# Optimization experiments

Measured on AMD Instinct MI355X. Metric: run time of the kernel, lower is better.

The kernel has to match this reference:

```python
import jax, jax.numpy as jnp
import numpy as np

B, I, H = 4096, 1024, 2048
EPS = 1e-5  # nn.GroupNorm default eps


def setup_inputs() -> dict:
    key = jax.random.key(0)
    ks = jax.random.split(key, 16)
    s_in = 1.0 / np.sqrt(I)
    s_h = 1.0 / np.sqrt(H)
    inp = {
        "x": jax.random.normal(ks[0], (B, I), jnp.float32),
        "h_prev": jax.random.normal(ks[1], (B, H), jnp.float32),
        "c_prev": jax.random.normal(ks[2], (B, H), jnp.float32),
        "n_prev": jnp.ones((B, H), jnp.float32),
        "m_prev": jax.random.normal(ks[3], (B, H), jnp.float32),
        # W_* : Linear(I, H) weight [H, I] + bias [H]
        "Wi": jax.random.uniform(ks[4], (H, I), jnp.float32, -s_in, s_in),
        "Wf": jax.random.uniform(ks[5], (H, I), jnp.float32, -s_in, s_in),
        "Wz": jax.random.uniform(ks[6], (H, I), jnp.float32, -s_in, s_in),
        "Wo": jax.random.uniform(ks[7], (H, I), jnp.float32, -s_in, s_in),
        "bi": jax.random.uniform(ks[8], (H,), jnp.float32, -s_in, s_in),
        "bf": jax.random.uniform(ks[9], (H,), jnp.float32, -s_in, s_in),
        "bz": jax.random.uniform(ks[10], (H,), jnp.float32, -s_in, s_in),
        "bo": jax.random.uniform(ks[11], (H,), jnp.float32, -s_in, s_in),
        # R_* : Linear(H, H, bias=False) weight [H, H]
        "Ri": jax.random.uniform(ks[12], (H, H), jnp.float32, -s_h, s_h),
        "Rf": jax.random.uniform(ks[13], (H, H), jnp.float32, -s_h, s_h),
        "Rz": jax.random.uniform(ks[14], (H, H), jnp.float32, -s_h, s_h),
        "Ro": jax.random.uniform(ks[15], (H, H), jnp.float32, -s_h, s_h),
        # GroupNorm(1, H) affine params
        "gn_w": jnp.ones((H,), jnp.float32),
        "gn_b": jnp.zeros((H,), jnp.float32),
    }
    return inp


def _group_norm1(x, w, b):
    # GroupNorm with 1 group on [B, H]: normalize over all H per sample
    mu = jnp.mean(x, axis=-1, keepdims=True)
    var = jnp.mean(jnp.square(x - mu), axis=-1, keepdims=True)
    return (x - mu) * jax.lax.rsqrt(var + EPS) * w + b


def reference(x, h_prev, c_prev, n_prev, m_prev,
              Wi, Wf, Wz, Wo, bi, bf, bz, bo,
              Ri, Rf, Rz, Ro, gn_w, gn_b):
    # Batch the 4 input and 4 recurrent GEMMs into one each: [B, 4H]
    Wcat = jnp.concatenate([Wi, Wf, Wz, Wo], axis=0)   # [4H, I]
    bcat = jnp.concatenate([bi, bf, bz, bo], axis=0)   # [4H]
    Rcat = jnp.concatenate([Ri, Rf, Rz, Ro], axis=0)   # [4H, H]
    pre = x @ Wcat.T + bcat + h_prev @ Rcat.T          # [B, 4H]
    pi, pf, pz, po = jnp.split(pre, 4, axis=-1)
    i = jax.nn.sigmoid(pi)
    f = jax.nn.sigmoid(pf)
    z = jnp.tanh(pz)
    o = jax.nn.sigmoid(po)
    m = jnp.maximum(f * m_prev, i)
    c = f * c_prev + i * z
    n = f * n_prev + i
    c_stab = c / n
    h = o * jnp.tanh(_group_norm1(c_stab, gn_w, gn_b))
    return (h, c, n, m)
```

## Files before the change

### kernel.cpp

```cpp
#include <hip/hip_runtime.h>
#include <hip/hip_bf16.h>
#include <math.h>

#define B_ 4096
#define I_ 1024
#define H_ 2048
#define K_ 3072
#define N4 8192
#define EPSGN 1e-5f

#define NT_K 48
#define PANB 16384
#define LDSB 65536

typedef __bf16 bf16;
typedef __bf16 bf16x8 __attribute__((ext_vector_type(8)));
typedef float  f32x4  __attribute__((ext_vector_type(4)));

__device__ __forceinline__ float sigm(float x) {
  return 1.0f / (1.0f + __expf(-x));
}
__device__ __forceinline__ float tanh_fast(float x) {
  float a = fabsf(x);
  float e = __expf(-2.0f * a);
  float t = (1.0f - e) / (1.0f + e);
  return copysignf(t, x);
}

__global__ void convA(const float* __restrict__ x, const float* __restrict__ hp,
                      char* __restrict__ At) {
  int sid = blockIdx.x * blockDim.x + threadIdx.x;
  int p = sid & 1023;
  int pan = sid >> 10;
  int mt = pan / 96;
  int rem = pan - mt * 96;
  int kt = rem >> 1;
  int h = rem & 1;
  int r = p >> 3;
  int ks = (p & 7) ^ (r & 7);
  int row = mt * 256 + h * 128 + r;
  int k = kt * 64 + ks * 8;
  const float* src = (k < I_) ? (x + (size_t)row * I_ + k)
                              : (hp + (size_t)row * H_ + (k - I_));
  f32x4 v0 = *(const f32x4*)src;
  f32x4 v1 = *(const f32x4*)(src + 4);
  bf16x8 o;
  o[0]=(bf16)v0[0]; o[1]=(bf16)v0[1]; o[2]=(bf16)v0[2]; o[3]=(bf16)v0[3];
  o[4]=(bf16)v1[0]; o[5]=(bf16)v1[1]; o[6]=(bf16)v1[2]; o[7]=(bf16)v1[3];
  *(bf16x8*)(At + (size_t)sid * 16) = o;
}

__global__ void convB(const float* __restrict__ Wi, const float* __restrict__ Wf,
                      const float* __restrict__ Wz, const float* __restrict__ Wo,
                      const float* __restrict__ Ri, const float* __restrict__ Rf,
                      const float* __restrict__ Rz, const float* __restrict__ Ro,
                      char* __restrict__ Bt) {
  int sid = blockIdx.x * blockDim.x + threadIdx.x;
  int p = sid & 1023;
  int pan = sid >> 10;
  int nt = pan / 96;
  int rem = pan - nt * 96;
  int kt = rem >> 1;
  int h = rem & 1;
  int r = p >> 3;
  int ks = (p & 7) ^ (r & 7);
  int n = nt * 256 + h * 128 + r;
  int g = n >> 11;
  int hr = n & 2047;
  int k = kt * 64 + ks * 8;
  const float* Wp = (g == 0) ? Wi : (g == 1) ? Wf : (g == 2) ? Wz : Wo;
  const float* Rp = (g == 0) ? Ri : (g == 1) ? Rf : (g == 2) ? Rz : Ro;
  const float* src = (k < I_) ? (Wp + (size_t)hr * I_ + k)
                              : (Rp + (size_t)hr * H_ + (k - I_));
  f32x4 v0 = *(const f32x4*)src;
  f32x4 v1 = *(const f32x4*)(src + 4);
  bf16x8 o;
  o[0]=(bf16)v0[0]; o[1]=(bf16)v0[1]; o[2]=(bf16)v0[2]; o[3]=(bf16)v0[3];
  o[4]=(bf16)v1[0]; o[5]=(bf16)v1[1]; o[6]=(bf16)v1[2]; o[7]=(bf16)v1[3];
  *(bf16x8*)(Bt + (size_t)sid * 16) = o;
}

__device__ __forceinline__ void gload16(const char* g, char* l) {
  __builtin_amdgcn_global_load_lds(
      (const __attribute__((address_space(1))) void*)g,
      (__attribute__((address_space(3))) void*)l, 16, 0, 0);
}
__device__ __forceinline__ void stage(const char* g, char* l) {
  gload16(g, l);
  gload16(g + 8192, l + 8192);
}

__global__ __launch_bounds__(512, 2) void gemm8(const char* __restrict__ At,
                                                const char* __restrict__ Bt,
                                                bf16* __restrict__ pre) {
  extern __shared__ char lds[];
  const int tid = threadIdx.x;
  const int lane = tid & 63;
  const int wv = tid >> 6;
  const int wm = wv >> 2;
  const int wn = wv & 3;

  int bid = (blockIdx.x & 7) * 64 + (blockIdx.x >> 3);
  const int bm = bid >> 5;
  const int bn = bid & 31;

  const char* a_src = At + (size_t)bm * (NT_K * 2 * PANB) + tid * 16;
  const char* b_src = Bt + (size_t)bn * (NT_K * 2 * PANB) + tid * 16;
  char* a_lds = lds + tid * 16;
  char* b_lds = lds + LDSB + tid * 16;

  const int l15 = lane & 15;
  const int l7  = lane & 7;
  const int q   = lane >> 4;
  int offk[2];
  offk[0] = l15 * 128 + (((0 + q) ^ l7) << 4);
  offk[1] = l15 * 128 + (((4 + q) ^ l7) << 4);

  const char* apan_base = lds + wm * PANB;
  const char* bpan_base = lds + LDSB + (wn >> 1) * PANB;
  const int bcol = (wn & 1) * 8192;

  f32x4 acc[8][4] = {};
  bf16x8 af[4][2], bfr[2][2][2];

  stage(b_src + 0 * PANB, b_lds + 0 * PANB);
  stage(b_src + 1 * PANB, b_lds + 1 * PANB);
  stage(a_src + 0 * PANB, a_lds + 0 * PANB);
  stage(a_src + 1 * PANB, a_lds + 1 * PANB);
  stage(b_src + 2 * PANB, b_lds + 2 * PANB);
  stage(b_src + 3 * PANB, b_lds + 3 * PANB);
  asm volatile("s_waitcnt vmcnt(4)" ::: "memory");
  __builtin_amdgcn_s_barrier();

#pragma unroll 2
  for (int t = 0; t < NT_K; ++t) {
    const int par = (t & 1) * 2;
    const char* apan = apan_base + par * PANB;
    const char* bpan = bpan_base + par * PANB;

#pragma unroll
    for (int fi = 0; fi < 4; ++fi)
#pragma unroll
      for (int ks = 0; ks < 2; ++ks)
        af[fi][ks] = *(const bf16x8*)(apan + fi * 2048 + offk[ks]);
#pragma unroll
    for (int fj = 0; fj < 2; ++fj)
#pragma unroll
      for (int ks = 0; ks < 2; ++ks)
        bfr[0][fj][ks] = *(const bf16x8*)(bpan + bcol + fj * 2048 + offk[ks]);
    if (t + 1 < NT_K)
      stage(a_src + (size_t)(t + 1) * 2 * PANB,
            a_lds + (((t + 1) & 1) * 2) * PANB);
    __builtin_amdgcn_s_barrier();
    asm volatile("s_waitcnt lgkmcnt(0)" ::: "memory");
    __builtin_amdgcn_s_setprio(1);
#pragma unroll
    for (int fi = 0; fi < 4; ++fi)
#pragma unroll
      for (int fj = 0; fj < 2; ++fj)
#pragma unroll
        for (int ks = 0; ks < 2; ++ks)
          acc[fi][fj] = __builtin_amdgcn_mfma_f32_16x16x32_bf16(
              af[fi][ks], bfr[0][fj][ks], acc[fi][fj], 0, 0, 0);
    __builtin_amdgcn_s_setprio(0);
    __builtin_amdgcn_s_barrier();

#pragma unroll
    for (int fj = 0; fj < 2; ++fj)
#pragma unroll
      for (int ks = 0; ks < 2; ++ks)
        bfr[1][fj][ks] = *(const bf16x8*)(bpan + bcol + 4096 + fj * 2048 + offk[ks]);
    if (t + 1 < NT_K)
      stage(a_src + (size_t)(t + 1) * 2 * PANB + PANB,
            a_lds + ((((t + 1) & 1) * 2) + 1) * PANB);
    __builtin_amdgcn_s_barrier();
    asm volatile("s_waitcnt lgkmcnt(0)" ::: "memory");
    __builtin_amdgcn_s_setprio(1);
#pragma unroll
    for (int fi = 0; fi < 4; ++fi)
#pragma unroll
      for (int fj = 0; fj < 2; ++fj)
#pragma unroll
        for (int ks = 0; ks < 2; ++ks)
          acc[fi][2 + fj] = __builtin_amdgcn_mfma_f32_16x16x32_bf16(
              af[fi][ks], bfr[1][fj][ks], acc[fi][2 + fj], 0, 0, 0);
    __builtin_amdgcn_s_setprio(0);
    __builtin_amdgcn_s_barrier();

#pragma unroll
    for (int fi = 0; fi < 4; ++fi)
#pragma unroll
      for (int ks = 0; ks < 2; ++ks)
        af[fi][ks] = *(const bf16x8*)(apan + 8192 + fi * 2048 + offk[ks]);
    if (t + 2 < NT_K)
      stage(b_src + (size_t)(t + 2) * 2 * PANB,
            b_lds + par * PANB);
    __builtin_amdgcn_s_barrier();
    asm volatile("s_waitcnt lgkmcnt(0)" ::: "memory");
    __builtin_amdgcn_s_setprio(1);
#pragma unroll
    for (int fi = 0; fi < 4; ++fi)
#pragma unroll
      for (int fj = 0; fj < 2; ++fj)
#pragma unroll
        for (int ks = 0; ks < 2; ++ks)
          acc[4 + fi][2 + fj] = __builtin_amdgcn_mfma_f32_16x16x32_bf16(
              af[fi][ks], bfr[1][fj][ks], acc[4 + fi][2 + fj], 0, 0, 0);
    __builtin_amdgcn_s_setprio(0);
    __builtin_amdgcn_s_barrier();

    if (t + 2 < NT_K)
      stage(b_src + (size_t)(t + 2) * 2 * PANB + PANB,
            b_lds + (par + 1) * PANB);
    __builtin_amdgcn_s_barrier();
    asm volatile("s_waitcnt lgkmcnt(0)" ::: "memory");
    __builtin_amdgcn_s_setprio(1);
#pragma unroll
    for (int fi = 0; fi < 4; ++fi)
#pragma unroll
      for (int fj = 0; fj < 2; ++fj)
#pragma unroll
        for (int ks = 0; ks < 2; ++ks)
          acc[4 + fi][fj] = __builtin_amdgcn_mfma_f32_16x16x32_bf16(
              af[fi][ks], bfr[0][fj][ks], acc[4 + fi][fj], 0, 0, 0);
    __builtin_amdgcn_s_setprio(0);
    if (t < NT_K - 2)
      asm volatile("s_waitcnt vmcnt(4)" ::: "memory");
    else
      asm volatile("s_waitcnt vmcnt(0)" ::: "memory");
    __builtin_amdgcn_s_barrier();
  }

  const int crow0 = (lane >> 4) * 4;
  const int ccol  = lane & 15;
#pragma unroll
  for (int mi = 0; mi < 8; ++mi)
#pragma unroll
    for (int nj = 0; nj < 4; ++nj)
#pragma unroll
      for (int j = 0; j < 4; ++j) {
        int row = bm * 256 + wm * 128 + mi * 16 + crow0 + j;
        int col = bn * 256 + wn * 64 + nj * 16 + ccol;
        pre[(size_t)row * N4 + col] = (bf16)acc[mi][nj][j];
      }
}

__global__ __launch_bounds__(256) void fusedpost(
    const bf16* __restrict__ pre,
    const float* __restrict__ bi, const float* __restrict__ bfp,
    const float* __restrict__ bz, const float* __restrict__ bo,
    const float* __restrict__ c_prev, const float* __restrict__ n_prev,
    const float* __restrict__ m_prev,
    const float* __restrict__ gnw, const float* __restrict__ gnb,
    float* __restrict__ out) {
  const int b = blockIdx.x;
  const int t = threadIdx.x;
  const int h0 = t * 8;
  const long PL = (long)B_ * H_;
  const long e = (long)b * H_ + h0;
  const bf16* prow = pre + (size_t)b * N4;

  bf16x8 PI = *(const bf16x8*)(prow + 0 * H_ + h0);
  bf16x8 PF = *(const bf16x8*)(prow + 1 * H_ + h0);
  bf16x8 PZ = *(const bf16x8*)(prow + 2 * H_ + h0);
  bf16x8 PO = *(const bf16x8*)(prow + 3 * H_ + h0);
  f32x4 BI0 = *(const f32x4*)(bi + h0),  BI1 = *(const f32x4*)(bi + h0 + 4);
  f32x4 BF0 = *(const f32x4*)(bfp + h0), BF1 = *(const f32x4*)(bfp + h0 + 4);
  f32x4 BZ0 = *(const f32x4*)(bz + h0),  BZ1 = *(const f32x4*)(bz + h0 + 4);
  f32x4 BO0 = *(const f32x4*)(bo + h0),  BO1 = *(const f32x4*)(bo + h0 + 4);
  f32x4 CP0 = *(const f32x4*)(c_prev + e), CP1 = *(const f32x4*)(c_prev + e + 4);
  f32x4 NP0 = *(const f32x4*)(n_prev + e), NP1 = *(const f32x4*)(n_prev + e + 4);
  f32x4 MP0 = *(const f32x4*)(m_prev + e), MP1 = *(const f32x4*)(m_prev + e + 4);

  float cs[8], og[8];
  f32x4 C0, C1, N0, N1, M0, M1;
  float sum = 0.f, sq = 0.f;
#pragma unroll
  for (int j = 0; j < 8; ++j) {
    float pi = (float)PI[j] + ((j < 4) ? BI0[j] : BI1[j - 4]);
    float pf = (float)PF[j] + ((j < 4) ? BF0[j] : BF1[j - 4]);
    float pz = (float)PZ[j] + ((j < 4) ? BZ0[j] : BZ1[j - 4]);
    float po = (float)PO[j] + ((j < 4) ? BO0[j] : BO1[j - 4]);
    float cp = (j < 4) ? CP0[j] : CP1[j - 4];
    float np = (j < 4) ? NP0[j] : NP1[j - 4];
    float mp = (j < 4) ? MP0[j] : MP1[j - 4];
    float ig = sigm(pi);
    float fg = sigm(pf);
    float zg = tanh_fast(pz);
    og[j] = sigm(po);
    float m = fmaxf(fg * mp, ig);
    float c = fg * cp + ig * zg;
    float n = fg * np + ig;
    if (j < 4) { C0[j] = c; N0[j] = n; M0[j] = m; }
    else       { C1[j-4] = c; N1[j-4] = n; M1[j-4] = m; }
    float v = c / n;
    cs[j] = v;
    sum += v;
    sq  += v * v;
  }
  *(f32x4*)(out + PL * 1 + e) = C0; *(f32x4*)(out + PL * 1 + e + 4) = C1;
  *(f32x4*)(out + PL * 2 + e) = N0; *(f32x4*)(out + PL * 2 + e + 4) = N1;
  *(f32x4*)(out + PL * 3 + e) = M0; *(f32x4*)(out + PL * 3 + e + 4) = M1;

#pragma unroll
  for (int off = 1; off < 64; off <<= 1) {
    sum += __shfl_xor(sum, off);
    sq  += __shfl_xor(sq, off);
  }
  __shared__ float s1[4], s2[4];
  const int wv = t >> 6, lane = t & 63;
  if (lane == 0) { s1[wv] = sum; s2[wv] = sq; }
  __syncthreads();
  sum = s1[0] + s1[1] + s1[2] + s1[3];
  sq  = s2[0] + s2[1] + s2[2] + s2[3];
  const float mu  = sum * (1.0f / H_);
  const float var = sq * (1.0f / H_) - mu * mu;
  const float rinv = rsqrtf(var + EPSGN);

  f32x4 GW0 = *(const f32x4*)(gnw + h0), GW1 = *(const f32x4*)(gnw + h0 + 4);
  f32x4 GB0 = *(const f32x4*)(gnb + h0), GB1 = *(const f32x4*)(gnb + h0 + 4);
  f32x4 Hh0, Hh1;
#pragma unroll
  for (int j = 0; j < 8; ++j) {
    float gw = (j < 4) ? GW0[j] : GW1[j - 4];
    float gb = (j < 4) ? GB0[j] : GB1[j - 4];
    float g = (cs[j] - mu) * rinv * gw + gb;
    float hv = og[j] * tanh_fast(g);
    if (j < 4) Hh0[j] = hv; else Hh1[j - 4] = hv;
  }
  *(f32x4*)(out + e) = Hh0;
  *(f32x4*)(out + e + 4) = Hh1;
}

extern "C" void kernel_launch(void* const* d_in, const int* in_sizes, int n_in,
                              void* d_out, int out_size, void* d_ws, size_t ws_size,
                              hipStream_t stream) {
  const float* x      = (const float*)d_in[0];
  const float* h_prev = (const float*)d_in[1];
  const float* c_prev = (const float*)d_in[2];
  const float* n_prev = (const float*)d_in[3];
  const float* m_prev = (const float*)d_in[4];
  const float* Wi = (const float*)d_in[5];
  const float* Wf = (const float*)d_in[6];
  const float* Wz = (const float*)d_in[7];
  const float* Wo = (const float*)d_in[8];
  const float* bi = (const float*)d_in[9];
  const float* bf = (const float*)d_in[10];
  const float* bz = (const float*)d_in[11];
  const float* bo = (const float*)d_in[12];
  const float* Ri = (const float*)d_in[13];
  const float* Rf = (const float*)d_in[14];
  const float* Rz = (const float*)d_in[15];
  const float* Ro = (const float*)d_in[16];
  const float* gnw = (const float*)d_in[17];
  const float* gnb = (const float*)d_in[18];

  char* ws = (char*)d_ws;
  char* At = ws;
  char* Bt = ws + (size_t)B_ * K_ * 2;
  bf16* pre = (bf16*)(ws + (size_t)B_ * K_ * 2 + (size_t)N4 * K_ * 2);
  float* out = (float*)d_out;

  hipFuncSetAttribute((const void*)gemm8,
                      hipFuncAttributeMaxDynamicSharedMemorySize, 131072);

  convA<<<((size_t)B_ * K_ / 8) / 256, 256, 0, stream>>>(x, h_prev, At);
  convB<<<((size_t)N4 * K_ / 8) / 256, 256, 0, stream>>>(Wi, Wf, Wz, Wo,
                                                         Ri, Rf, Rz, Ro, Bt);
  gemm8<<<512, 512, 131072, stream>>>(At, Bt, pre);
  fusedpost<<<B_, 256, 0, stream>>>(pre, bi, bf, bz, bo,
                                    c_prev, n_prev, m_prev, gnw, gnb, out);
}
```

Baseline: 290.1 us.

## Software-pipeline LDS fragment loads behind MFMA clusters and halve barriers per k-tile

Restructures the GEMM main loop so the LDS-to-register fragment loads for the next quadrant are issued right after each MFMA cluster and are consumed only after the following barrier. The first fragments are preloaded before the loop, and the next tile's A and B0 fragments are prefetched at the end of each iteration. This removes the explicit lgkmcnt(0) waits, cuts barriers from eight to four per k-tile, and loosens the vmcnt wait. The aim is to hide LDS latency under matrix math, at the cost of more live registers and tighter reliance on correct ordering for buffer reuse.

Result: no change. 286.8 us (-1.1%).

```diff
diff --git a/kernel.cpp b/kernel.cpp
--- a/kernel.cpp
+++ b/kernel.cpp
@@ -121,7 +121,9 @@
   const int bcol = (wn & 1) * 8192;
 
   f32x4 acc[8][4] = {};
-  bf16x8 af[4][2], bfr[2][2][2];
+  bf16x8 af[4][2];
+  bf16x8 bn0[2][2];
+  bf16x8 bn1[2][2];
 
   stage(b_src + 0 * PANB, b_lds + 0 * PANB);
   stage(b_src + 1 * PANB, b_lds + 1 * PANB);
@@ -132,102 +134,105 @@
   asm volatile("s_waitcnt vmcnt(4)" ::: "memory");
   __builtin_amdgcn_s_barrier();
 
+#pragma unroll
+  for (int mi = 0; mi < 4; ++mi)
+#pragma unroll
+    for (int ks = 0; ks < 2; ++ks)
+      af[mi][ks] = *(const bf16x8*)(apan_base + mi * 2048 + offk[ks]);
+#pragma unroll
+  for (int nj = 0; nj < 2; ++nj)
+#pragma unroll
+    for (int ks = 0; ks < 2; ++ks)
+      bn0[nj][ks] = *(const bf16x8*)(bpan_base + bcol + nj * 2048 + offk[ks]);
+
 #pragma unroll 2
   for (int t = 0; t < NT_K; ++t) {
     const int par = (t & 1) * 2;
-    const char* apan = apan_base + par * PANB;
-    const char* bpan = bpan_base + par * PANB;
-
-#pragma unroll
-    for (int fi = 0; fi < 4; ++fi)
+    const char* apan  = apan_base + par * PANB;
+    const char* bpan  = bpan_base + par * PANB;
+    const char* apanN = apan_base + (2 - par) * PANB;
+    const char* bpanN = bpan_base + (2 - par) * PANB;
+
+    __builtin_amdgcn_s_setprio(1);
+#pragma unroll
+    for (int mi = 0; mi < 4; ++mi)
+#pragma unroll
+      for (int nj = 0; nj < 2; ++nj)
+#pragma unroll
+        for (int ks = 0; ks < 2; ++ks)
+          acc[mi][nj] = __builtin_amdgcn_mfma_f32_16x16x32_bf16(
+              af[mi][ks], bn0[nj][ks], acc[mi][nj], 0, 0, 0);
+    __builtin_amdgcn_s_setprio(0);
+    if (t + 1 < NT_K)
+      stage(a_src + (size_t)(t + 1) * 2 * PANB, a_lds + (2 - par) * PANB);
+#pragma unroll
+    for (int nj = 0; nj < 2; ++nj)
 #pragma unroll
       for (int ks = 0; ks < 2; ++ks)
-        af[fi][ks] = *(const bf16x8*)(apan + fi * 2048 + offk[ks]);
-#pragma unroll
-    for (int fj = 0; fj < 2; ++fj)
+        bn1[nj][ks] = *(const bf16x8*)(bpan + bcol + 4096 + nj * 2048 + offk[ks]);
+    __builtin_amdgcn_s_barrier();
+
+    __builtin_amdgcn_s_setprio(1);
+#pragma unroll
+    for (int mi = 0; mi < 4; ++mi)
+#pragma unroll
+      for (int nj = 0; nj < 2; ++nj)
+#pragma unroll
+        for (int ks = 0; ks < 2; ++ks)
+          acc[mi][2 + nj] = __builtin_amdgcn_mfma_f32_16x16x32_bf16(
+              af[mi][ks], bn1[nj][ks], acc[mi][2 + nj], 0, 0, 0);
+    __builtin_amdgcn_s_setprio(0);
+    if (t + 1 < NT_K)
+      stage(a_src + (size_t)(t + 1) * 2 * PANB + PANB, a_lds + (3 - par) * PANB);
+#pragma unroll
+    for (int mi = 0; mi < 4; ++mi)
 #pragma unroll
       for (int ks = 0; ks < 2; ++ks)
-        bfr[0][fj][ks] = *(const bf16x8*)(bpan + bcol + fj * 2048 + offk[ks]);
-    if (t + 1 < NT_K)
-      stage(a_src + (size_t)(t + 1) * 2 * PANB,
-            a_lds + (((t + 1) & 1) * 2) * PANB);
+        af[mi][ks] = *(const bf16x8*)(apan + 8192 + mi * 2048 + offk[ks]);
     __builtin_amdgcn_s_barrier();
-    asm volatile("s_waitcnt lgkmcnt(0)" ::: "memory");
+
     __builtin_amdgcn_s_setprio(1);
 #pragma unroll
-    for (int fi = 0; fi < 4; ++fi)
-#pragma unroll
-      for (int fj = 0; fj < 2; ++fj)
-#pragma unroll
-        for (int ks = 0; ks < 2; ++ks)
-          acc[fi][fj] = __builtin_amdgcn_mfma_f32_16x16x32_bf16(
-              af[fi][ks], bfr[0][fj][ks], acc[fi][fj], 0, 0, 0);
+    for (int mi = 0; mi < 4; ++mi)
+#pragma unroll
+      for (int nj = 0; nj < 2; ++nj)
+#pragma unroll
+        for (int ks = 0; ks < 2; ++ks)
+          acc[4 + mi][2 + nj] = __builtin_amdgcn_mfma_f32_16x16x32_bf16(
+              af[mi][ks], bn1[nj][ks], acc[4 + mi][2 + nj], 0, 0, 0);
     __builtin_amdgcn_s_setprio(0);
-    __builtin_amdgcn_s_barrier();
-
-#pragma unroll
-    for (int fj = 0; fj < 2; ++fj)
-#pragma unroll
-      for (int ks = 0; ks < 2; ++ks)
-        bfr[1][fj][ks] = *(const bf16x8*)(bpan + bcol + 4096 + fj * 2048 + offk[ks]);
-    if (t + 1 < NT_K)
-      stage(a_src + (size_t)(t + 1) * 2 * PANB + PANB,
-            a_lds + ((((t + 1) & 1) * 2) + 1) * PANB);
-    __builtin_amdgcn_s_barrier();
-    asm volatile("s_waitcnt lgkmcnt(0)" ::: "memory");
-    __builtin_amdgcn_s_setprio(1);
-#pragma unroll
-    for (int fi = 0; fi < 4; ++fi)
-#pragma unroll
-      for (int fj = 0; fj < 2; ++fj)
-#pragma unroll
-        for (int ks = 0; ks < 2; ++ks)
-          acc[fi][2 + fj] = __builtin_amdgcn_mfma_f32_16x16x32_bf16(
-              af[fi][ks], bfr[1][fj][ks], acc[fi][2 + fj], 0, 0, 0);
-    __builtin_amdgcn_s_setprio(0);
-    __builtin_amdgcn_s_barrier();
-
-#pragma unroll
-    for (int fi = 0; fi < 4; ++fi)
-#pragma unroll
-      for (int ks = 0; ks < 2; ++ks)
-        af[fi][ks] = *(const bf16x8*)(apan + 8192 + fi * 2048 + offk[ks]);
     if (t + 2 < NT_K)
-      stage(b_src + (size_t)(t + 2) * 2 * PANB,
-            b_lds + par * PANB);
-    __builtin_amdgcn_s_barrier();
-    asm volatile("s_waitcnt lgkmcnt(0)" ::: "memory");
-    __builtin_amdgcn_s_setprio(1);
-#pragma unroll
-    for (int fi = 0; fi < 4; ++fi)
-#pragma unroll
-      for (int fj = 0; fj < 2; ++fj)
-#pragma unroll
-        for (int ks = 0; ks < 2; ++ks)
-          acc[4 + fi][2 + fj] = __builtin_amdgcn_mfma_f32_16x16x32_bf16(
-              af[fi][ks], bfr[1][fj][ks], acc[4 + fi][2 + fj], 0, 0, 0);
-    __builtin_amdgcn_s_setprio(0);
-    __builtin_amdgcn_s_barrier();
-
-    if (t + 2 < NT_K)
-      stage(b_src + (size_t)(t + 2) * 2 * PANB + PANB,
-            b_lds + (par + 1) * PANB);
-    __builtin_amdgcn_s_barrier();
-    asm volatile("s_waitcnt lgkmcnt(0)" ::: "memory");
-    __builtin_amdgcn_s_setprio(1);
-#pragma unroll
-    for (int fi = 0; fi < 4; ++fi)
-#pragma unroll
-      for (int fj = 0; fj < 2; ++fj)
-#pragma unroll
-        for (int ks = 0; ks < 2; ++ks)
-          acc[4 + fi][fj] = __builtin_amdgcn_mfma_f32_16x16x32_bf16(
-              af[fi][ks], bfr[0][fj][ks], acc[4 + fi][fj], 0, 0, 0);
-    __builtin_amdgcn_s_setprio(0);
+      stage(b_src + (size_t)(t + 2) * 2 * PANB, b_lds + par * PANB);
     if (t < NT_K - 2)
-      asm volatile("s_waitcnt vmcnt(4)" ::: "memory");
+      asm volatile("s_waitcnt vmcnt(2)" ::: "memory");
     else
       asm volatile("s_waitcnt vmcnt(0)" ::: "memory");
+    __builtin_amdgcn_s_barrier();
+
+    __builtin_amdgcn_s_setprio(1);
+#pragma unroll
+    for (int mi = 0; mi < 4; ++mi)
+#pragma unroll
+      for (int nj = 0; nj < 2; ++nj)
+#pragma unroll
+        for (int ks = 0; ks < 2; ++ks)
+          acc[4 + mi][nj] = __builtin_amdgcn_mfma_f32_16x16x32_bf16(
+              af[mi][ks], bn0[nj][ks], acc[4 + mi][nj], 0, 0, 0);
+    __builtin_amdgcn_s_setprio(0);
+    if (t + 2 < NT_K)
+      stage(b_src + (size_t)(t + 2) * 2 * PANB + PANB, b_lds + (par + 1) * PANB);
+    if (t + 1 < NT_K) {
+#pragma unroll
+      for (int mi = 0; mi < 4; ++mi)
+#pragma unroll
+        for (int ks = 0; ks < 2; ++ks)
+          af[mi][ks] = *(const bf16x8*)(apanN + mi * 2048 + offk[ks]);
+#pragma unroll
+      for (int nj = 0; nj < 2; ++nj)
+#pragma unroll
+        for (int ks = 0; ks < 2; ++ks)
+          bn0[nj][ks] = *(const bf16x8*)(bpanN + bcol + nj * 2048 + offk[ks]);
+    }
     __builtin_amdgcn_s_barrier();
   }
 
```
